# Performance work log

Measured on AMD Instinct MI355X. Metric: run time of the kernel, lower is better.

Reference implementation:

```python
import jax, jax.numpy as jnp
import numpy as np

HOURS = 24
SU, SL, TU, TL = 100.0, 0.0, 100.0, 0.0
N, M, L, E = 32, 128, 128, 128
T_DIM, U_DIM, L_DIM = 25, 2000, 10000


def setup_inputs() -> dict:
    key = jax.random.key(0)
    ks = jax.random.split(key, 18)
    s = 0.02
    full_seq = jax.random.randint(ks[0], (N, M), 1, L_DIM)
    time_seq = jax.random.randint(ks[1], (N, M), 1, 720)
    user = jax.random.randint(ks[2], (N,), 1, U_DIM)
    posneg = jax.random.randint(ks[3], (N, L), 1, L_DIM)
    traj_len = jax.random.randint(ks[4], (N,), 1, M + 1)
    mat1 = jax.random.uniform(ks[5], (N, M, M, 2), dtype=jnp.float32) * 100.0
    mat2 = jax.random.uniform(ks[6], (N, M, L), dtype=jnp.float32) * 100.0
    vec = jax.random.uniform(ks[7], (N, M), dtype=jnp.float32) * 100.0
    def tab(k, n):  # embedding table with padding_idx=0 zeroed
        return (jax.random.normal(k, (n, E), dtype=jnp.float32) * s).at[0].set(0.0)
    emb_t = tab(ks[8], T_DIM)
    emb_u = tab(ks[9], U_DIM)
    emb_loc = tab(ks[10], L_DIM)
    emb_sl = tab(ks[11], 2)
    emb_su = tab(ks[12], 2)
    emb_tl = tab(ks[13], 2)
    emb_tu = tab(ks[14], 2)
    Wq = jax.random.normal(ks[15], (E, E), dtype=jnp.float32) * s
    Wk = jax.random.normal(ks[16], (E, E), dtype=jnp.float32) * s
    Wv = jax.random.normal(ks[17], (E, E), dtype=jnp.float32) * s
    return dict(full_seq=full_seq, time_seq=time_seq, user=user, posneg=posneg,
                traj_len=traj_len, mat1=mat1, mat2=mat2, vec=vec,
                emb_t=emb_t, emb_u=emb_u, emb_loc=emb_loc,
                emb_sl=emb_sl, emb_su=emb_su, emb_tl=emb_tl, emb_tu=emb_tu,
                Wq=Wq, Wk=Wk, Wv=Wv)


def _interval(e_l, e_u, d, lo, hi):
    # (e_l*(hi-d) + e_u*(d-lo)) / (hi-lo); e_* are [...,E], d is [...]
    return (e_l * (hi - d)[..., None] + e_u * (d - lo)[..., None]) / (hi - lo)


def reference(full_seq, time_seq, user, posneg, traj_len, mat1, mat2, vec,
              emb_t, emb_u, emb_loc, emb_sl, emb_su, emb_tl, emb_tu, Wq, Wk, Wv):
    n, m = full_seq.shape
    tim = (time_seq - 1) % HOURS + 1
    joint = emb_t[tim] + emb_loc[full_seq] + emb_u[user][:, None, :]  # [N,M,E]

    # --- stage 1: self-attention with spatiotemporal relative bias ---
    delta_s, delta_t = mat1[..., 0], mat1[..., 1]  # [N,M,M]
    valid = (jnp.arange(m)[None, :] < traj_len[:, None]).astype(jnp.int32)  # [N,M]
    mask2d = valid[:, None, :] * valid[:, :, None]  # [N,M,M] in {0,1}
    delta = (_interval(emb_sl[mask2d], emb_su[mask2d], delta_s, SL, SU)
             + _interval(emb_tl[mask2d], emb_tu[mask2d], delta_t, TL, TU)).sum(-1)
    fmask = mask2d.astype(joint.dtype)
    q = joint @ Wq.T
    k = joint @ Wk.T
    v = joint @ Wv.T
    attn = jax.nn.softmax(jnp.einsum('bme,bne->bmn', q, k) + delta, axis=-1) * fmask
    self_attn = jnp.einsum('bmn,bne->bme', attn, v)  # [N,M,E]

    # --- stage 2: candidate attention ---
    mask1 = valid[:, :, None]  # [N,M,1]
    sp = _interval(emb_sl[mask1], emb_su[mask1], mat2, SL, SU)            # [N,M,L,E]
    tm = _interval(emb_tl[mask1], emb_tu[mask1], vec[:, :, None], TL, TU)  # [N,M,1,E]
    self_delta = jnp.swapaxes((sp + tm).sum(-1), -1, -2)  # [N,L,M]
    cand = emb_loc[posneg]  # [N,L,E]
    attn2 = jnp.einsum('ble,bme->blm', cand, self_attn) * self_delta
    return attn2.sum(-1)  # [N,L]
```

## Files before the change

### kernel.cpp

```cpp
#include <hip/hip_runtime.h>
#include <hip/hip_bf16.h>

#define HOURS 24
#define MM 128
#define EE 128
#define PS 136

typedef short bf16x8 __attribute__((ext_vector_type(8)));
typedef float f32x4 __attribute__((ext_vector_type(4)));

__device__ __forceinline__ unsigned short f2bfu(float f) {
    __hip_bfloat16 h = __float2bfloat16(f);
    return __builtin_bit_cast(unsigned short, h);
}
__device__ __forceinline__ float bfu2f(unsigned short u) {
    unsigned int x = ((unsigned int)u) << 16;
    return __builtin_bit_cast(float, x);
}
__device__ __forceinline__ unsigned int pack2(float a, float b) {
    return (unsigned int)f2bfu(a) | ((unsigned int)f2bfu(b) << 16);
}
__device__ __forceinline__ int swz8(int row, int unit) {
    return row * 128 + (((unit ^ (row & 7)) & 15) << 3);
}
__device__ __forceinline__ bf16x8 load_w_frag(const float* base) {
    float4 x = *(const float4*)base;
    float4 y = *(const float4*)(base + 4);
    union { unsigned int u[4]; bf16x8 v; } r;
    r.u[0] = pack2(x.x, x.y); r.u[1] = pack2(x.z, x.w);
    r.u[2] = pack2(y.x, y.y); r.u[3] = pack2(y.z, y.w);
    return r.v;
}

#define MFMA(a, b, c) __builtin_amdgcn_mfma_f32_16x16x32_bf16(a, b, c, 0, 0, 0)

__global__ __launch_bounds__(256) void k_one(
    const int* __restrict__ full_seq, const int* __restrict__ time_seq,
    const int* __restrict__ user, const int* __restrict__ posneg,
    const int* __restrict__ traj_len,
    const float* __restrict__ mat1, const float* __restrict__ mat2,
    const float* __restrict__ vecg,
    const float* __restrict__ emb_t, const float* __restrict__ emb_u,
    const float* __restrict__ emb_loc,
    const float* __restrict__ esl, const float* __restrict__ esu,
    const float* __restrict__ etl, const float* __restrict__ etu,
    const float* __restrict__ Wq, const float* __restrict__ Wk,
    const float* __restrict__ Wv,
    float* __restrict__ outp)
{
    __shared__ alignas(16) short U0[MM * PS];
    __shared__ alignas(16) short Kl[MM * EE];
    __shared__ alignas(16) short Vl[MM * EE];
    __shared__ alignas(16) short Ql[MM * EE];
    __shared__ alignas(16) short CAl[16 * EE];
    __shared__ alignas(16) short CVh[16 * PS];
    __shared__ alignas(16) short CVm[16 * PS];
    __shared__ float tms[MM], bsv[MM], coef[8], PART[4][16];

    const int b = blockIdx.y, lc = blockIdx.x;
    const int l0g = lc * 16;
    const int tid = threadIdx.x;
    const int w = tid >> 6, l = tid & 63;
    const int lr = l & 15, lg = l >> 4;
    const int tl = traj_len[b];

    {
        const float* tb4[4] = {esl, esu, etl, etu};
#pragma unroll
        for (int s = 0; s < 2; ++s) {
            int c = 2 * w + s;
            const float* t = tb4[c >> 1];
            float v = t[(c & 1) * 128 + l] + t[(c & 1) * 128 + 64 + l];
#pragma unroll
            for (int off = 32; off >= 1; off >>= 1) v += __shfl_xor(v, off, 64);
            if (l == 0) coef[c] = v;
        }
    }
    {
        int uid = user[b];
        const float4* Eu4 = (const float4*)(emb_u + (size_t)uid * 128);
#pragma unroll
        for (int it = 0; it < 16; ++it) {
            int i4 = it * 256 + tid;
            int mm = i4 >> 5, fq = i4 & 31;
            int t = time_seq[b * MM + mm];
            int tim = (t - 1) % HOURS + 1;
            int loc = full_seq[b * MM + mm];
            float4 a = ((const float4*)(emb_t + (size_t)tim * 128))[fq];
            float4 c = ((const float4*)(emb_loc + (size_t)loc * 128))[fq];
            float4 u = Eu4[fq];
            uint2 pk;
            pk.x = pack2(a.x + c.x + u.x, a.y + c.y + u.y);
            pk.y = pack2(a.z + c.z + u.z, a.w + c.w + u.w);
            *(uint2*)&U0[swz8(mm, fq >> 1) + (fq & 1) * 4] = pk;
        }
#pragma unroll
        for (int it = 0; it < 2; ++it) {
            int u = it * 256 + tid;
            int row = u >> 5, fq = u & 31;
            int p = posneg[b * MM + l0g + row];
            float4 v = ((const float4*)(emb_loc + (size_t)p * 128))[fq];
            uint2 pk;
            pk.x = pack2(v.x, v.y);
            pk.y = pack2(v.z, v.w);
            *(uint2*)&CAl[swz8(row, fq >> 1) + (fq & 1) * 4] = pk;
        }
    }
    __syncthreads();

    if (tid < 128) {
        int vv = (tid < tl) ? 1 : 0;
        float ssl = vv ? coef[1] : coef[0];
        float ssu = vv ? coef[3] : coef[2];
        float stl = vv ? coef[5] : coef[4];
        float stu = vv ? coef[7] : coef[6];
        tms[tid] = ssl + stl + (stu - stl) * 0.01f * vecg[b * MM + tid];
        bsv[tid] = (ssu - ssl) * 0.01f;
    }
    {
        const float* Ws[3] = {Wk, Wv, Wq};
        short* Xs[3] = {Kl, Vl, Ql};
#pragma unroll
        for (int g = 0; g < 3; ++g) {
            const float* W = Ws[g];
            short* X = Xs[g];
            bf16x8 af[2][4];
#pragma unroll
            for (int nt = 0; nt < 2; ++nt) {
                int n = (2 * w + nt) * 16 + lr;
#pragma unroll
                for (int kf = 0; kf < 4; ++kf)
                    af[nt][kf] = load_w_frag(W + (size_t)n * 128 + kf * 32 + lg * 8);
            }
#pragma unroll
            for (int mt = 0; mt < 8; ++mt) {
                bf16x8 bj[4];
#pragma unroll
                for (int kf = 0; kf < 4; ++kf)
                    bj[kf] = *(const bf16x8*)&U0[swz8(mt * 16 + lr, kf * 4 + lg)];
                f32x4 a0 = (f32x4){0.f,0.f,0.f,0.f}, a1 = (f32x4){0.f,0.f,0.f,0.f};
#pragma unroll
                for (int kf = 0; kf < 4; ++kf) {
                    a0 = MFMA(af[0][kf], bj[kf], a0);
                    a1 = MFMA(af[1][kf], bj[kf], a1);
                }
                int m = mt * 16 + lr;
#pragma unroll
                for (int nt = 0; nt < 2; ++nt) {
                    f32x4 av = nt ? a1 : a0;
                    int n0 = (2 * w + nt) * 16 + lg * 4;
                    uint2 pk;
                    pk.x = pack2(av[0], av[1]);
                    pk.y = pack2(av[2], av[3]);
                    *(uint2*)&X[swz8(m, n0 >> 3) + (n0 & 7)] = pk;
                }
            }
        }
    }
    __syncthreads();

    {
        bf16x8 ca[4];
#pragma unroll
        for (int kf = 0; kf < 4; ++kf)
            ca[kf] = *(const bf16x8*)&CAl[swz8(lr, kf * 4 + lg)];
#pragma unroll
        for (int t2 = 0; t2 < 2; ++t2) {
            int jt = 2 * w + t2;
            f32x4 acc = (f32x4){0.f,0.f,0.f,0.f};
#pragma unroll
            for (int kf = 0; kf < 4; ++kf) {
                bf16x8 bv = *(const bf16x8*)&Vl[swz8(jt * 16 + lr, kf * 4 + lg)];
                acc = MFMA(ca[kf], bv, acc);
            }
#pragma unroll
            for (int r = 0; r < 4; ++r) {
                float f = acc[r];
                unsigned short h = f2bfu(f);
                float rem = f - bfu2f(h);
                CVh[(4 * lg + r) * PS + jt * 16 + lr] = (short)h;
                CVm[(4 * lg + r) * PS + jt * 16 + lr] = (short)f2bfu(rem);
            }
        }
    }
    {
        float c0_1 = coef[1] + coef[5];
        float c1_1 = (coef[3] - coef[1]) * 0.01f;
        float c2_1 = (coef[7] - coef[5]) * 0.01f;
        float c0_0 = coef[0] + coef[4];
        float c1_0 = (coef[2] - coef[0]) * 0.01f;
        float c2_0 = (coef[6] - coef[4]) * 0.01f;
#pragma unroll
        for (int t2 = 0; t2 < 2; ++t2) {
            int it = 2 * w + t2;
            bf16x8 qf[4];
#pragma unroll
            for (int kf = 0; kf < 4; ++kf)
                qf[kf] = *(const bf16x8*)&Ql[swz8(it * 16 + lr, kf * 4 + lg)];
            f32x4 acc[8];
#pragma unroll
            for (int jt = 0; jt < 8; ++jt) acc[jt] = (f32x4){0.f,0.f,0.f,0.f};
#pragma unroll
            for (int jt = 0; jt < 8; ++jt) {
#pragma unroll
                for (int kf = 0; kf < 4; ++kf) {
                    bf16x8 bk = *(const bf16x8*)&Kl[swz8(jt * 16 + lr, kf * 4 + lg)];
                    acc[jt] = MFMA(qf[kf], bk, acc[jt]);
                }
            }
#pragma unroll
            for (int r = 0; r < 4; ++r) {
                int ig = it * 16 + 4 * lg + r;
                int mi = (ig < tl) ? 1 : 0;
                float lgv[8];
                int mk[8];
#pragma unroll
                for (int jt = 0; jt < 8; ++jt) {
                    int j = jt * 16 + lr;
                    mk[jt] = mi & ((j < tl) ? 1 : 0);
                    float2 d = *(const float2*)&mat1[((size_t)(b * MM + ig) * MM + j) * 2];
                    float cc0 = mk[jt] ? c0_1 : c0_0;
                    float cc1 = mk[jt] ? c1_1 : c1_0;
                    float cc2 = mk[jt] ? c2_1 : c2_0;
                    lgv[jt] = acc[jt][r] + cc0 + cc1 * d.x + cc2 * d.y;
                }
                float mx = lgv[0];
#pragma unroll
                for (int jt = 1; jt < 8; ++jt) mx = fmaxf(mx, lgv[jt]);
#pragma unroll
                for (int off = 8; off >= 1; off >>= 1) mx = fmaxf(mx, __shfl_xor(mx, off, 64));
                float ee[8], sum = 0.f;
#pragma unroll
                for (int jt = 0; jt < 8; ++jt) { ee[jt] = __expf(lgv[jt] - mx); sum += ee[jt]; }
#pragma unroll
                for (int off = 8; off >= 1; off >>= 1) sum += __shfl_xor(sum, off, 64);
                float inv = 1.0f / sum;
#pragma unroll
                for (int jt = 0; jt < 8; ++jt)
                    U0[ig * PS + jt * 16 + lr] = (short)f2bfu(ee[jt] * inv * (float)mk[jt]);
            }
        }
    }
    __syncthreads();

    {
        bf16x8 cah[4], cam[4];
#pragma unroll
        for (int kf = 0; kf < 4; ++kf) {
            cah[kf] = *(const bf16x8*)&CVh[lr * PS + kf * 32 + lg * 8];
            cam[kf] = *(const bf16x8*)&CVm[lr * PS + kf * 32 + lg * 8];
        }
        float val[4] = {0.f, 0.f, 0.f, 0.f};
#pragma unroll
        for (int t2 = 0; t2 < 2; ++t2) {
            int mt = 2 * w + t2;
            f32x4 acc = (f32x4){0.f,0.f,0.f,0.f};
#pragma unroll
            for (int kf = 0; kf < 4; ++kf) {
                bf16x8 bp = *(const bf16x8*)&U0[(mt * 16 + lr) * PS + kf * 32 + lg * 8];
                acc = MFMA(cah[kf], bp, acc);
                acc = MFMA(cam[kf], bp, acc);
            }
            int m = mt * 16 + lr;
            float4 m2 = *(const float4*)&mat2[(size_t)(b * MM + m) * MM + l0g + lg * 4];
            float wt = tms[m], wb = bsv[m];
            val[0] += acc[0] * (wt + wb * m2.x);
            val[1] += acc[1] * (wt + wb * m2.y);
            val[2] += acc[2] * (wt + wb * m2.z);
            val[3] += acc[3] * (wt + wb * m2.w);
        }
#pragma unroll
        for (int r = 0; r < 4; ++r) {
            float v = val[r];
            v += __shfl_xor(v, 1, 64);
            v += __shfl_xor(v, 2, 64);
            v += __shfl_xor(v, 4, 64);
            v += __shfl_xor(v, 8, 64);
            if (lr == 0) PART[w][lg * 4 + r] = v;
        }
    }
    __syncthreads();
    if (tid < 16)
        outp[b * MM + l0g + tid] = PART[0][tid] + PART[1][tid] + PART[2][tid] + PART[3][tid];
}

extern "C" void kernel_launch(void* const* d_in, const int* in_sizes, int n_in,
                              void* d_out, int out_size, void* d_ws, size_t ws_size,
                              hipStream_t stream) {
    const int* full_seq = (const int*)d_in[0];
    const int* time_seq = (const int*)d_in[1];
    const int* user     = (const int*)d_in[2];
    const int* posneg   = (const int*)d_in[3];
    const int* traj_len = (const int*)d_in[4];
    const float* mat1   = (const float*)d_in[5];
    const float* mat2   = (const float*)d_in[6];
    const float* vec    = (const float*)d_in[7];
    const float* emb_t  = (const float*)d_in[8];
    const float* emb_u  = (const float*)d_in[9];
    const float* emb_loc= (const float*)d_in[10];
    const float* emb_sl = (const float*)d_in[11];
    const float* emb_su = (const float*)d_in[12];
    const float* emb_tl = (const float*)d_in[13];
    const float* emb_tu = (const float*)d_in[14];
    const float* Wq     = (const float*)d_in[15];
    const float* Wk     = (const float*)d_in[16];
    const float* Wv     = (const float*)d_in[17];

    k_one<<<dim3(8, 32), 256, 0, stream>>>(full_seq, time_seq, user, posneg, traj_len,
                                           mat1, mat2, vec, emb_t, emb_u, emb_loc,
                                           emb_sl, emb_su, emb_tl, emb_tu,
                                           Wq, Wk, Wv, (float*)d_out);
}
```

Before: 25.80 us.

## Precompute Wq^T·Wk and Wv^T in prep kernel, reassociate attention products

Adds a small prep kernel that forms the fused weight product A = Wk^T·Wq (bf16) and a transposed Wv in workspace. The main kernel computes scores as J·A·J^T and projects candidates through Wv before multiplying by J, so it no longer builds separate Q, K and V matrices per block. Block size goes from 256 to 512 threads. This removes redundant per-block QKV projections and shared memory, at the cost of an extra launch and an extra bf16 rounding of the fused weight product.

After: 27.75 us. 7.5% more time.

```diff
diff --git a/kernel.cpp b/kernel.cpp
--- a/kernel.cpp
+++ b/kernel.cpp
@@ -4,7 +4,6 @@
 #define HOURS 24
 #define MM 128
 #define EE 128
-#define PS 136
 
 typedef short bf16x8 __attribute__((ext_vector_type(8)));
 typedef float f32x4 __attribute__((ext_vector_type(4)));
@@ -22,6 +21,9 @@
 }
 __device__ __forceinline__ int swz8(int row, int unit) {
     return row * 128 + (((unit ^ (row & 7)) & 15) << 3);
+}
+__device__ __forceinline__ int swzs(int row, int col) {
+    return row * 128 + ((((col >> 3) ^ (row & 7)) & 15) << 3) + (col & 7);
 }
 __device__ __forceinline__ bf16x8 load_w_frag(const float* base) {
     float4 x = *(const float4*)base;
@@ -34,7 +36,56 @@
 
 #define MFMA(a, b, c) __builtin_amdgcn_mfma_f32_16x16x32_bf16(a, b, c, 0, 0, 0)
 
-__global__ __launch_bounds__(256) void k_one(
+__global__ __launch_bounds__(256) void k_prep(
+    const float* __restrict__ Wq, const float* __restrict__ Wk,
+    const float* __restrict__ Wv,
+    short* __restrict__ ATws, short* __restrict__ WvTws)
+{
+    __shared__ alignas(16) short WqTl[128 * 128];
+    __shared__ alignas(16) short WkTl[16 * 128];
+    int f0 = blockIdx.x * 16;
+    int tid = threadIdx.x;
+#pragma unroll 4
+    for (int it = 0; it < 64; ++it) {
+        int idx = it * 256 + tid;
+        int n = idx >> 7, e = idx & 127;
+        WqTl[swzs(e, n)] = (short)f2bfu(Wq[n * 128 + e]);
+    }
+#pragma unroll
+    for (int it = 0; it < 8; ++it) {
+        int idx = it * 256 + tid;
+        int n = idx >> 4, j = idx & 15;
+        WkTl[swzs(j, n)] = (short)f2bfu(Wk[n * 128 + f0 + j]);
+    }
+#pragma unroll
+    for (int it = 0; it < 8; ++it) {
+        int idx = it * 256 + tid;
+        int j = idx >> 7, e = idx & 127;
+        WvTws[(f0 + j) * 128 + e] = (short)f2bfu(Wv[e * 128 + f0 + j]);
+    }
+    __syncthreads();
+    int l = tid & 63, w = tid >> 6;
+    int lr = l & 15, lg = l >> 4;
+    bf16x8 af[4];
+#pragma unroll
+    for (int kf = 0; kf < 4; ++kf)
+        af[kf] = *(const bf16x8*)&WkTl[swz8(lr, kf * 4 + lg)];
+#pragma unroll
+    for (int t2 = 0; t2 < 2; ++t2) {
+        int et = 2 * w + t2;
+        f32x4 acc = (f32x4){0.f, 0.f, 0.f, 0.f};
+#pragma unroll
+        for (int kf = 0; kf < 4; ++kf) {
+            bf16x8 bf = *(const bf16x8*)&WqTl[swz8(et * 16 + lr, kf * 4 + lg)];
+            acc = MFMA(af[kf], bf, acc);
+        }
+#pragma unroll
+        for (int r = 0; r < 4; ++r)
+            ATws[(f0 + lg * 4 + r) * 128 + et * 16 + lr] = (short)f2bfu(acc[r]);
+    }
+}
+
+__global__ __launch_bounds__(512) void k_main(
     const int* __restrict__ full_seq, const int* __restrict__ time_seq,
     const int* __restrict__ user, const int* __restrict__ posneg,
     const int* __restrict__ traj_len,
@@ -44,21 +95,17 @@
     const float* __restrict__ emb_loc,
     const float* __restrict__ esl, const float* __restrict__ esu,
     const float* __restrict__ etl, const float* __restrict__ etu,
-    const float* __restrict__ Wq, const float* __restrict__ Wk,
-    const float* __restrict__ Wv,
+    const short* __restrict__ ATws, const short* __restrict__ WvTws,
     float* __restrict__ outp)
 {
-    __shared__ alignas(16) short U0[MM * PS];
-    __shared__ alignas(16) short Kl[MM * EE];
-    __shared__ alignas(16) short Vl[MM * EE];
-    __shared__ alignas(16) short Ql[MM * EE];
-    __shared__ alignas(16) short CAl[16 * EE];
-    __shared__ alignas(16) short CVh[16 * PS];
-    __shared__ alignas(16) short CVm[16 * PS];
-    __shared__ float tms[MM], bsv[MM], coef[8], PART[4][16];
-
-    const int b = blockIdx.y, lc = blockIdx.x;
-    const int l0g = lc * 16;
+    __shared__ alignas(16) short Jl[128 * 128];
+    __shared__ alignas(16) short T1l[128 * 128];
+    __shared__ alignas(16) short CWl[16 * 128];
+    __shared__ alignas(16) short CVh[16 * 128];
+    __shared__ alignas(16) short CVm[16 * 128];
+    __shared__ float tms[128], bsv[128], coef[8], PART[8][16];
+
+    const int b = blockIdx.y, l0g = blockIdx.x * 16;
     const int tid = threadIdx.x;
     const int w = tid >> 6, l = tid & 63;
     const int lr = l & 15, lg = l >> 4;
@@ -66,22 +113,19 @@
 
     {
         const float* tb4[4] = {esl, esu, etl, etu};
-#pragma unroll
-        for (int s = 0; s < 2; ++s) {
-            int c = 2 * w + s;
-            const float* t = tb4[c >> 1];
-            float v = t[(c & 1) * 128 + l] + t[(c & 1) * 128 + 64 + l];
-#pragma unroll
-            for (int off = 32; off >= 1; off >>= 1) v += __shfl_xor(v, off, 64);
-            if (l == 0) coef[c] = v;
-        }
+        const float* t = tb4[w >> 1];
+        int row = w & 1;
+        float v = t[row * 128 + l] + t[row * 128 + 64 + l];
+#pragma unroll
+        for (int off = 32; off >= 1; off >>= 1) v += __shfl_xor(v, off, 64);
+        if (l == 0) coef[w] = v;
     }
     {
         int uid = user[b];
         const float4* Eu4 = (const float4*)(emb_u + (size_t)uid * 128);
 #pragma unroll
-        for (int it = 0; it < 16; ++it) {
-            int i4 = it * 256 + tid;
+        for (int it = 0; it < 8; ++it) {
+            int i4 = it * 512 + tid;
             int mm = i4 >> 5, fq = i4 & 31;
             int t = time_seq[b * MM + mm];
             int tim = (t - 1) % HOURS + 1;
@@ -92,18 +136,7 @@
             uint2 pk;
             pk.x = pack2(a.x + c.x + u.x, a.y + c.y + u.y);
             pk.y = pack2(a.z + c.z + u.z, a.w + c.w + u.w);
-            *(uint2*)&U0[swz8(mm, fq >> 1) + (fq & 1) * 4] = pk;
-        }
-#pragma unroll
-        for (int it = 0; it < 2; ++it) {
-            int u = it * 256 + tid;
-            int row = u >> 5, fq = u & 31;
-            int p = posneg[b * MM + l0g + row];
-            float4 v = ((const float4*)(emb_loc + (size_t)p * 128))[fq];
-            uint2 pk;
-            pk.x = pack2(v.x, v.y);
-            pk.y = pack2(v.z, v.w);
-            *(uint2*)&CAl[swz8(row, fq >> 1) + (fq & 1) * 4] = pk;
+            *(uint2*)&Jl[swz8(mm, fq >> 1) + (fq & 1) * 4] = pk;
         }
     }
     __syncthreads();
@@ -118,71 +151,78 @@
         bsv[tid] = (ssu - ssl) * 0.01f;
     }
     {
-        const float* Ws[3] = {Wk, Wv, Wq};
-        short* Xs[3] = {Kl, Vl, Ql};
-#pragma unroll
-        for (int g = 0; g < 3; ++g) {
-            const float* W = Ws[g];
-            short* X = Xs[g];
-            bf16x8 af[2][4];
-#pragma unroll
-            for (int nt = 0; nt < 2; ++nt) {
-                int n = (2 * w + nt) * 16 + lr;
-#pragma unroll
-                for (int kf = 0; kf < 4; ++kf)
-                    af[nt][kf] = load_w_frag(W + (size_t)n * 128 + kf * 32 + lg * 8);
+        bf16x8 atf[4];
+#pragma unroll
+        for (int kf = 0; kf < 4; ++kf)
+            atf[kf] = *(const bf16x8*)&ATws[(w * 16 + lr) * 128 + kf * 32 + lg * 8];
+        int n0 = w * 16 + lg * 4;
+#pragma unroll
+        for (int mt = 0; mt < 8; ++mt) {
+            f32x4 acc = (f32x4){0.f, 0.f, 0.f, 0.f};
+#pragma unroll
+            for (int kf = 0; kf < 4; ++kf) {
+                bf16x8 bj = *(const bf16x8*)&Jl[swz8(mt * 16 + lr, kf * 4 + lg)];
+                acc = MFMA(atf[kf], bj, acc);
             }
-#pragma unroll
-            for (int mt = 0; mt < 8; ++mt) {
-                bf16x8 bj[4];
-#pragma unroll
-                for (int kf = 0; kf < 4; ++kf)
-                    bj[kf] = *(const bf16x8*)&U0[swz8(mt * 16 + lr, kf * 4 + lg)];
-                f32x4 a0 = (f32x4){0.f,0.f,0.f,0.f}, a1 = (f32x4){0.f,0.f,0.f,0.f};
-#pragma unroll
-                for (int kf = 0; kf < 4; ++kf) {
-                    a0 = MFMA(af[0][kf], bj[kf], a0);
-                    a1 = MFMA(af[1][kf], bj[kf], a1);
-                }
-                int m = mt * 16 + lr;
-#pragma unroll
-                for (int nt = 0; nt < 2; ++nt) {
-                    f32x4 av = nt ? a1 : a0;
-                    int n0 = (2 * w + nt) * 16 + lg * 4;
-                    uint2 pk;
-                    pk.x = pack2(av[0], av[1]);
-                    pk.y = pack2(av[2], av[3]);
-                    *(uint2*)&X[swz8(m, n0 >> 3) + (n0 & 7)] = pk;
-                }
+            uint2 pk;
+            pk.x = pack2(acc[0], acc[1]);
+            pk.y = pack2(acc[2], acc[3]);
+            *(uint2*)&T1l[swz8(mt * 16 + lr, n0 >> 3) + (n0 & 7)] = pk;
+        }
+        int p = posneg[b * MM + l0g + lr];
+        bf16x8 ca[4], wvf[4];
+#pragma unroll
+        for (int kf = 0; kf < 4; ++kf) {
+            ca[kf] = load_w_frag(emb_loc + (size_t)p * 128 + kf * 32 + lg * 8);
+            wvf[kf] = *(const bf16x8*)&WvTws[(w * 16 + lr) * 128 + kf * 32 + lg * 8];
+        }
+        f32x4 accw = (f32x4){0.f, 0.f, 0.f, 0.f};
+#pragma unroll
+        for (int kf = 0; kf < 4; ++kf) accw = MFMA(ca[kf], wvf[kf], accw);
+#pragma unroll
+        for (int r = 0; r < 4; ++r)
+            CWl[swzs(lg * 4 + r, w * 16 + lr)] = (short)f2bfu(accw[r]);
+    }
+    __syncthreads();
+
+    f32x4 sacc[8];
+    {
+        bf16x8 t1f[4];
+#pragma unroll
+        for (int kf = 0; kf < 4; ++kf)
+            t1f[kf] = *(const bf16x8*)&T1l[swz8(w * 16 + lr, kf * 4 + lg)];
+#pragma unroll
+        for (int jt = 0; jt < 8; ++jt) sacc[jt] = (f32x4){0.f, 0.f, 0.f, 0.f};
+#pragma unroll
+        for (int jt = 0; jt < 8; ++jt)
+#pragma unroll
+            for (int kf = 0; kf < 4; ++kf) {
+                bf16x8 bj = *(const bf16x8*)&Jl[swz8(jt * 16 + lr, kf * 4 + lg)];
+                sacc[jt] = MFMA(t1f[kf], bj, sacc[jt]);
             }
-        }
-    }
-    __syncthreads();
-
-    {
-        bf16x8 ca[4];
+    }
+    {
+        bf16x8 cwf[4];
 #pragma unroll
         for (int kf = 0; kf < 4; ++kf)
-            ca[kf] = *(const bf16x8*)&CAl[swz8(lr, kf * 4 + lg)];
-#pragma unroll
-        for (int t2 = 0; t2 < 2; ++t2) {
-            int jt = 2 * w + t2;
-            f32x4 acc = (f32x4){0.f,0.f,0.f,0.f};
-#pragma unroll
-            for (int kf = 0; kf < 4; ++kf) {
-                bf16x8 bv = *(const bf16x8*)&Vl[swz8(jt * 16 + lr, kf * 4 + lg)];
-                acc = MFMA(ca[kf], bv, acc);
-            }
-#pragma unroll
-            for (int r = 0; r < 4; ++r) {
-                float f = acc[r];
-                unsigned short h = f2bfu(f);
-                float rem = f - bfu2f(h);
-                CVh[(4 * lg + r) * PS + jt * 16 + lr] = (short)h;
-                CVm[(4 * lg + r) * PS + jt * 16 + lr] = (short)f2bfu(rem);
-            }
-        }
-    }
+            cwf[kf] = *(const bf16x8*)&CWl[swz8(lr, kf * 4 + lg)];
+        f32x4 accv = (f32x4){0.f, 0.f, 0.f, 0.f};
+#pragma unroll
+        for (int kf = 0; kf < 4; ++kf) {
+            bf16x8 bj = *(const bf16x8*)&Jl[swz8(w * 16 + lr, kf * 4 + lg)];
+            accv = MFMA(cwf[kf], bj, accv);
+        }
+#pragma unroll
+        for (int r = 0; r < 4; ++r) {
+            float f = accv[r];
+            unsigned short h = f2bfu(f);
+            float rem = f - bfu2f(h);
+            CVh[swzs(lg * 4 + r, w * 16 + lr)] = (short)h;
+            CVm[swzs(lg * 4 + r, w * 16 + lr)] = (short)f2bfu(rem);
+        }
+    }
+    __syncthreads();
+
     {
         float c0_1 = coef[1] + coef[5];
         float c1_1 = (coef[3] - coef[1]) * 0.01f;
@@ -191,84 +231,61 @@
         float c1_0 = (coef[2] - coef[0]) * 0.01f;
         float c2_0 = (coef[6] - coef[4]) * 0.01f;
 #pragma unroll
-        for (int t2 = 0; t2 < 2; ++t2) {
-            int it = 2 * w + t2;
-            bf16x8 qf[4];
-#pragma unroll
-            for (int kf = 0; kf < 4; ++kf)
-                qf[kf] = *(const bf16x8*)&Ql[swz8(it * 16 + lr, kf * 4 + lg)];
-            f32x4 acc[8];
-#pragma unroll
-            for (int jt = 0; jt < 8; ++jt) acc[jt] = (f32x4){0.f,0.f,0.f,0.f};
+        for (int r = 0; r < 4; ++r) {
+            int ig = w * 16 + lg * 4 + r;
+            int mi = (ig < tl) ? 1 : 0;
+            float lgv[8];
+            int mk[8];
 #pragma unroll
             for (int jt = 0; jt < 8; ++jt) {
-#pragma unroll
-                for (int kf = 0; kf < 4; ++kf) {
-                    bf16x8 bk = *(const bf16x8*)&Kl[swz8(jt * 16 + lr, kf * 4 + lg)];
-                    acc[jt] = MFMA(qf[kf], bk, acc[jt]);
-                }
+                int j = jt * 16 + lr;
+                mk[jt] = mi & ((j < tl) ? 1 : 0);
+                float2 d = *(const float2*)&mat1[((size_t)(b * MM + ig) * MM + j) * 2];
+                float cc0 = mk[jt] ? c0_1 : c0_0;
+                float cc1 = mk[jt] ? c1_1 : c1_0;
+                float cc2 = mk[jt] ? c2_1 : c2_0;
+                lgv[jt] = sacc[jt][r] + cc0 + cc1 * d.x + cc2 * d.y;
             }
-#pragma unroll
-            for (int r = 0; r < 4; ++r) {
-                int ig = it * 16 + 4 * lg + r;
-                int mi = (ig < tl) ? 1 : 0;
-                float lgv[8];
-                int mk[8];
-#pragma unroll
-                for (int jt = 0; jt < 8; ++jt) {
-                    int j = jt * 16 + lr;
-                    mk[jt] = mi & ((j < tl) ? 1 : 0);
-                    float2 d = *(const float2*)&mat1[((size_t)(b * MM + ig) * MM + j) * 2];
-                    float cc0 = mk[jt] ? c0_1 : c0_0;
-                    float cc1 = mk[jt] ? c1_1 : c1_0;
-                    float cc2 = mk[jt] ? c2_1 : c2_0;
-                    lgv[jt] = acc[jt][r] + cc0 + cc1 * d.x + cc2 * d.y;
-                }
-                float mx = lgv[0];
-#pragma unroll
-                for (int jt = 1; jt < 8; ++jt) mx = fmaxf(mx, lgv[jt]);
-#pragma unroll
-                for (int off = 8; off >= 1; off >>= 1) mx = fmaxf(mx, __shfl_xor(mx, off, 64));
-                float ee[8], sum = 0.f;
-#pragma unroll
-                for (int jt = 0; jt < 8; ++jt) { ee[jt] = __expf(lgv[jt] - mx); sum += ee[jt]; }
-#pragma unroll
-                for (int off = 8; off >= 1; off >>= 1) sum += __shfl_xor(sum, off, 64);
-                float inv = 1.0f / sum;
-#pragma unroll
-                for (int jt = 0; jt < 8; ++jt)
-                    U0[ig * PS + jt * 16 + lr] = (short)f2bfu(ee[jt] * inv * (float)mk[jt]);
-            }
-        }
-    }
-    __syncthreads();
-
-    {
-        bf16x8 cah[4], cam[4];
-#pragma unroll
-        for (int kf = 0; kf < 4; ++kf) {
-            cah[kf] = *(const bf16x8*)&CVh[lr * PS + kf * 32 + lg * 8];
-            cam[kf] = *(const bf16x8*)&CVm[lr * PS + kf * 32 + lg * 8];
-        }
-        float val[4] = {0.f, 0.f, 0.f, 0.f};
-#pragma unroll
-        for (int t2 = 0; t2 < 2; ++t2) {
-            int mt = 2 * w + t2;
-            f32x4 acc = (f32x4){0.f,0.f,0.f,0.f};
-#pragma unroll
-            for (int kf = 0; kf < 4; ++kf) {
-                bf16x8 bp = *(const bf16x8*)&U0[(mt * 16 + lr) * PS + kf * 32 + lg * 8];
-                acc = MFMA(cah[kf], bp, acc);
-                acc = MFMA(cam[kf], bp, acc);
-            }
-            int m = mt * 16 + lr;
-            float4 m2 = *(const float4*)&mat2[(size_t)(b * MM + m) * MM + l0g + lg * 4];
-            float wt = tms[m], wb = bsv[m];
-            val[0] += acc[0] * (wt + wb * m2.x);
-            val[1] += acc[1] * (wt + wb * m2.y);
-            val[2] += acc[2] * (wt + wb * m2.z);
-            val[3] += acc[3] * (wt + wb * m2.w);
-        }
+            float mx = lgv[0];
+#pragma unroll
+            for (int jt = 1; jt < 8; ++jt) mx = fmaxf(mx, lgv[jt]);
+#pragma unroll
+            for (int off = 8; off >= 1; off >>= 1) mx = fmaxf(mx, __shfl_xor(mx, off, 64));
+            float ee[8], sum = 0.f;
+#pragma unroll
+            for (int jt = 0; jt < 8; ++jt) { ee[jt] = __expf(lgv[jt] - mx); sum += ee[jt]; }
+#pragma unroll
+            for (int off = 8; off >= 1; off >>= 1) sum += __shfl_xor(sum, off, 64);
+            float inv = 1.0f / sum;
+#pragma unroll
+            for (int jt = 0; jt < 8; ++jt)
+                Jl[swzs(ig, jt * 16 + lr)] = (short)f2bfu(ee[jt] * inv * (float)mk[jt]);
+        }
+    }
+    __syncthreads();
+
+    {
+        bf16x8 cvh[4], cvm[4], bp[4];
+#pragma unroll
+        for (int kf = 0; kf < 4; ++kf) {
+            cvh[kf] = *(const bf16x8*)&CVh[swz8(lr, kf * 4 + lg)];
+            cvm[kf] = *(const bf16x8*)&CVm[swz8(lr, kf * 4 + lg)];
+            bp[kf]  = *(const bf16x8*)&Jl[swz8(w * 16 + lr, kf * 4 + lg)];
+        }
+        f32x4 acc = (f32x4){0.f, 0.f, 0.f, 0.f};
+#pragma unroll
+        for (int kf = 0; kf < 4; ++kf) {
+            acc = MFMA(cvh[kf], bp[kf], acc);
+            acc = MFMA(cvm[kf], bp[kf], acc);
+        }
+        int i = w * 16 + lr;
+        float4 m2 = *(const float4*)&mat2[(size_t)(b * MM + i) * MM + l0g + lg * 4];
+        float wt = tms[i], wb = bsv[i];
+        float val[4];
+        val[0] = acc[0] * (wt + wb * m2.x);
+        val[1] = acc[1] * (wt + wb * m2.y);
+        val[2] = acc[2] * (wt + wb * m2.z);
+        val[3] = acc[3] * (wt + wb * m2.w);
 #pragma unroll
         for (int r = 0; r < 4; ++r) {
             float v = val[r];
@@ -280,8 +297,12 @@
         }
     }
     __syncthreads();
-    if (tid < 16)
-        outp[b * MM + l0g + tid] = PART[0][tid] + PART[1][tid] + PART[2][tid] + PART[3][tid];
+    if (tid < 16) {
+        float s = 0.f;
+#pragma unroll
+        for (int w8 = 0; w8 < 8; ++w8) s += PART[w8][tid];
+        outp[b * MM + l0g + tid] = s;
+    }
 }
 
 extern "C" void kernel_launch(void* const* d_in, const int* in_sizes, int n_in,
@@ -306,8 +327,12 @@
     const float* Wk     = (const float*)d_in[16];
     const float* Wv     = (const float*)d_in[17];
 
-    k_one<<<dim3(8, 32), 256, 0, stream>>>(full_seq, time_seq, user, posneg, traj_len,
-                                           mat1, mat2, vec, emb_t, emb_u, emb_loc,
-                                           emb_sl, emb_su, emb_tl, emb_tu,
-                                           Wq, Wk, Wv, (float*)d_out);
-}
+    short* ATws  = (short*)d_ws;
+    short* WvTws = ATws + 128 * 128;
+
+    k_prep<<<8, 256, 0, stream>>>(Wq, Wk, Wv, ATws, WvTws);
+    k_main<<<dim3(8, 32), 512, 0, stream>>>(full_seq, time_seq, user, posneg, traj_len,
+                                            mat1, mat2, vec, emb_t, emb_u, emb_loc,
+                                            emb_sl, emb_su, emb_tl, emb_tu,
+                                            ATws, WvTws, (float*)d_out);
+}
```
